# Performance work log

Hardware: AMD Instinct MI355X
Metric: run time of the kernel (lower is better)

## Reference

```python
import jax, jax.numpy as jnp
import numpy as np

B, N, L, K, C1 = 128, 300, 600, 19, 100  # batch, num_cnns, input_length, filter_size, fc hidden
PS = 7  # pool size == stride
LC = L - (K - 1)               # 582, conv output length
LP = (LC - PS) // PS + 1       # 83, pooled length
NC = 2                         # num_classes
EPS = 1e-5


def _bn(x, g, b, m, v):
    # eval-mode batchnorm, params broadcast along given axes already
    return g * (x - m) * jax.lax.rsqrt(v + EPS) + b


def setup_inputs() -> dict:
    key = jax.random.key(0)
    ks = jax.random.split(key, 20)
    f = lambda i, shape, s=0.1: (jax.random.normal(ks[i], shape, dtype=jnp.float32) * s)
    pv = lambda i, shape: (jax.random.uniform(ks[i], shape, dtype=jnp.float32) + 0.5)
    return {
        'x': jax.random.normal(ks[0], (B, 4, L), dtype=jnp.float32),
        'conv_w': f(1, (N, 4, K)), 'conv_b': f(2, (N,)),
        'bn1_g': pv(3, (N,)), 'bn1_b': f(4, (N,)), 'bn1_m': f(5, (N,)), 'bn1_v': pv(6, (N,)),
        'fc1_w': f(7, (N, C1, LP)), 'fc1_b': f(8, (N, C1)),
        'bn2_g': pv(9, (N, C1)), 'bn2_b': f(10, (N, C1)), 'bn2_m': f(11, (N, C1)), 'bn2_v': pv(12, (N, C1)),
        'fc2_w': f(13, (N, C1)), 'fc2_b': f(14, (N,)),
        'bn3_g': pv(15, (N,)), 'bn3_b': f(16, (N,)), 'bn3_m': f(17, (N,)), 'bn3_v': pv(18, (N,)),
        'final_w': f(19, (NC, N)), 'final_b': jnp.zeros((NC,), dtype=jnp.float32),
    }


def reference(x, conv_w, conv_b, bn1_g, bn1_b, bn1_m, bn1_v,
              fc1_w, fc1_b, bn2_g, bn2_b, bn2_m, bn2_v,
              fc2_w, fc2_b, bn3_g, bn3_b, bn3_m, bn3_v,
              final_w, final_b):
    # grouped conv on a repeated input == plain conv with 4 in-channels, N out-channels
    h = jax.lax.conv_general_dilated(x, conv_w, window_strides=(1,), padding='VALID',
                                     dimension_numbers=('NCH', 'OIH', 'NCH'))  # [B,N,582]
    h = h + conv_b[None, :, None]
    h = _bn(h, bn1_g[None, :, None], bn1_b[None, :, None], bn1_m[None, :, None], bn1_v[None, :, None])
    h = jnp.exp(h)
    # MaxPool1d(7,7): [B,N,582] -> [B,N,83]
    h = jax.lax.reduce_window(h, -jnp.inf, jax.lax.max,
                              window_dimensions=(1, 1, PS), window_strides=(1, 1, PS), padding='VALID')
    # grouped 1x1 conv == per-unit dense: [B,N,83] x [N,100,83] -> [B,N,100]
    h = jnp.einsum('bnp,nhp->bnh', h, fc1_w) + fc1_b[None]
    h = jax.nn.relu(_bn(h, bn2_g[None], bn2_b[None], bn2_m[None], bn2_v[None]))
    # second grouped 1x1 conv: [B,N,100] x [N,100] -> [B,N]
    h = jnp.einsum('bnh,nh->bn', h, fc2_w) + fc2_b[None]
    h = jax.nn.relu(_bn(h, bn3_g[None], bn3_b[None], bn3_m[None], bn3_v[None]))
    return h @ final_w.T + final_b  # [B,num_classes]
```

## Files before the change

kernel.cpp:

```cpp
#include <hip/hip_runtime.h>
#include <math.h>

#define EPS_ 1e-5f

__global__ __launch_bounds__(256) void kP(const float* __restrict__ fc1w,
                                          const float* __restrict__ conv_w,
                                          float* __restrict__ w1Tp,
                                          float* __restrict__ cw4) {
    const int blk = blockIdx.x, tid = threadIdx.x;
    if (blk < 300) {
        __shared__ float sm[83 * 101];
        for (int i = tid; i < 8300; i += 256) {
            const int h = i / 83, p = i - h * 83;
            sm[p * 101 + h] = fc1w[(size_t)blk * 8300 + i];
        }
        __syncthreads();
        for (int i = tid; i < 9296; i += 256) {
            const int p = i / 112, h = i - p * 112;
            w1Tp[(size_t)blk * 9296 + i] = (h < 100) ? sm[p * 101 + h] : 0.f;
        }
    } else {
        const int cq = blk - 300;
        const int c  = cq / 5;
        const int kq = cq - c * 5;
        for (int n = tid; n < 300; n += 256) {
            float4 v;
            const int k0 = 4 * kq;
            v.x = (k0 + 0 < 19) ? conv_w[n * 76 + c * 19 + k0 + 0] : 0.f;
            v.y = (k0 + 1 < 19) ? conv_w[n * 76 + c * 19 + k0 + 1] : 0.f;
            v.z = (k0 + 2 < 19) ? conv_w[n * 76 + c * 19 + k0 + 2] : 0.f;
            v.w = (k0 + 3 < 19) ? conv_w[n * 76 + c * 19 + k0 + 3] : 0.f;
            reinterpret_cast<float4*>(cw4)[(c * 5 + kq) * 300 + n] = v;
        }
    }
}

__global__ __launch_bounds__(64) void kA(
        const float* __restrict__ x,
        const float* __restrict__ cw4,
        const float* __restrict__ conv_b,
        const float* __restrict__ g1, const float* __restrict__ b1,
        const float* __restrict__ m1, const float* __restrict__ v1,
        float* __restrict__ pooled)
{
    const int id  = blockIdx.x;
    const int b   = id / 112;
    const int sub = id - b * 112;
    if (sub >= 105) return;
    const int ng  = sub / 21;
    const int pc  = sub - ng * 21;
    const int p0c = pc * 4;
    const int p0  = (p0c > 79) ? 79 : p0c;
    const int lane = threadIdx.x;
    const int n   = ng * 64 + lane;
    const int nc  = (n < 300) ? n : 299;

    const float4* w4 = reinterpret_cast<const float4*>(cw4);

    float acc[28];
    #pragma unroll
    for (int i = 0; i < 28; ++i) acc[i] = 0.f;

    #pragma unroll 1
    for (int c = 0; c < 4; ++c) {
        const float* xc = x + b * 2400 + c * 600 + 7 * p0;
        float xw[46];
        #pragma unroll
        for (int j = 0; j < 46; ++j) xw[j] = xc[j];
        #pragma unroll
        for (int kq = 0; kq < 5; ++kq) {
            const float4 wv = w4[(c * 5 + kq) * 300 + nc];
            const int ni = (kq == 4) ? 3 : 4;
            #pragma unroll
            for (int i = 0; i < ni; ++i) {
                const int k = 4 * kq + i;
                const float wvv = (i == 0) ? wv.x : (i == 1) ? wv.y
                                : (i == 2) ? wv.z : wv.w;
                #pragma unroll
                for (int p = 0; p < 4; ++p)
                    #pragma unroll
                    for (int q = 0; q < 7; ++q)
                        acc[p * 7 + q] = fmaf(xw[7 * p + q + k], wvv,
                                              acc[p * 7 + q]);
            }
        }
    }

    const float A1 = g1[nc] * rsqrtf(v1[nc] + EPS_);
    const float B1 = fmaf(A1, conv_b[nc] - m1[nc], b1[nc]);
    if (n < 300) {
        float* op = pooled + ((size_t)n * 83 + p0) * 128 + b;
        #pragma unroll
        for (int p = 0; p < 4; ++p) {
            float mx = -INFINITY;
            #pragma unroll
            for (int q = 0; q < 7; ++q)
                mx = fmaxf(mx, fmaf(A1, acc[p * 7 + q], B1));
            op[p * 128] = __expf(mx);
        }
    }
}

__global__ __launch_bounds__(256, 2) void kB(
        const float* __restrict__ pooled,
        const float* __restrict__ w1Tp,
        const float* __restrict__ fc1b,
        const float* __restrict__ g2, const float* __restrict__ b2,
        const float* __restrict__ m2, const float* __restrict__ v2,
        const float* __restrict__ fc2w,
        const float* __restrict__ fc2b,
        const float* __restrict__ g3, const float* __restrict__ b3,
        const float* __restrict__ m3, const float* __restrict__ v3,
        float* __restrict__ sout)
{
    __shared__ __align__(16) float sW[83 * 112];
    __shared__ float2 sRed[4][64];
    const int n   = blockIdx.x;
    const int tid = threadIdx.x;

    {
        const float4* src = reinterpret_cast<const float4*>(w1Tp + (size_t)n * 9296);
        float4* dst = reinterpret_cast<float4*>(sW);
        for (int i = tid; i < 2324; i += 256) dst[i] = src[i];
    }
    __syncthreads();

    const int lane = tid & 63;
    const int wv   = __builtin_amdgcn_readfirstlane(tid >> 6);
    const int h0   = wv * 28;
    const int b0   = lane * 2;

    const float* pp = pooled + (size_t)n * 83 * 128 + b0;

    float acc[28][2];
    #pragma unroll
    for (int j = 0; j < 28; ++j) { acc[j][0] = 0.f; acc[j][1] = 0.f; }

    #pragma unroll 4
    for (int p = 0; p < 83; ++p) {
        const float2 pv = *reinterpret_cast<const float2*>(pp + p * 128);
        const float* wrow = sW + p * 112 + h0;
        #pragma unroll
        for (int jq = 0; jq < 7; ++jq) {
            const float4 w = *reinterpret_cast<const float4*>(wrow + 4 * jq);
            acc[jq * 4 + 0][0] = fmaf(w.x, pv.x, acc[jq * 4 + 0][0]);
            acc[jq * 4 + 0][1] = fmaf(w.x, pv.y, acc[jq * 4 + 0][1]);
            acc[jq * 4 + 1][0] = fmaf(w.y, pv.x, acc[jq * 4 + 1][0]);
            acc[jq * 4 + 1][1] = fmaf(w.y, pv.y, acc[jq * 4 + 1][1]);
            acc[jq * 4 + 2][0] = fmaf(w.z, pv.x, acc[jq * 4 + 2][0]);
            acc[jq * 4 + 2][1] = fmaf(w.z, pv.y, acc[jq * 4 + 2][1]);
            acc[jq * 4 + 3][0] = fmaf(w.w, pv.x, acc[jq * 4 + 3][0]);
            acc[jq * 4 + 3][1] = fmaf(w.w, pv.y, acc[jq * 4 + 3][1]);
        }
    }

    const int nh = (wv < 3) ? 28 : 16;
    float p0s = 0.f, p1s = 0.f;
    for (int j = 0; j < nh; ++j) {
        const int hi = n * 100 + h0 + j;
        const float A2 = g2[hi] * rsqrtf(v2[hi] + EPS_);
        const float C2 = fmaf(A2, fc1b[hi] - m2[hi], b2[hi]);
        const float w2 = fc2w[hi];
        p0s = fmaf(fmaxf(fmaf(A2, acc[j][0], C2), 0.f), w2, p0s);
        p1s = fmaf(fmaxf(fmaf(A2, acc[j][1], C2), 0.f), w2, p1s);
    }
    sRed[wv][lane] = make_float2(p0s, p1s);
    __syncthreads();

    if (tid < 128) {
        const int l = tid >> 1, r = tid & 1;
        float s = (r == 0)
            ? (sRed[0][l].x + sRed[1][l].x + sRed[2][l].x + sRed[3][l].x)
            : (sRed[0][l].y + sRed[1][l].y + sRed[2][l].y + sRed[3][l].y);
        s += fc2b[n];
        const float A3 = g3[n] * rsqrtf(v3[n] + EPS_);
        const float z = fmaf(A3, s - m3[n], b3[n]);
        sout[n * 128 + tid] = fmaxf(z, 0.f);
    }
}

__global__ __launch_bounds__(64) void kC(
        const float* __restrict__ sout,
        const float* __restrict__ fw,
        const float* __restrict__ fb,
        float* __restrict__ out)
{
    const int b = blockIdx.x, t = threadIdx.x;
    float a0 = 0.f, a1 = 0.f;
    for (int nn = t; nn < 300; nn += 64) {
        const float v = sout[nn * 128 + b];
        a0 = fmaf(v, fw[nn], a0);
        a1 = fmaf(v, fw[300 + nn], a1);
    }
    #pragma unroll
    for (int off = 32; off > 0; off >>= 1) {
        a0 += __shfl_xor(a0, off, 64);
        a1 += __shfl_xor(a1, off, 64);
    }
    if (t == 0) {
        out[b * 2 + 0] = a0 + fb[0];
        out[b * 2 + 1] = a1 + fb[1];
    }
}

extern "C" void kernel_launch(void* const* d_in, const int* in_sizes, int n_in,
                              void* d_out, int out_size, void* d_ws, size_t ws_size,
                              hipStream_t stream) {
    const float* x      = (const float*)d_in[0];
    const float* conv_w = (const float*)d_in[1];
    const float* conv_b = (const float*)d_in[2];
    const float* g1 = (const float*)d_in[3];
    const float* b1 = (const float*)d_in[4];
    const float* m1 = (const float*)d_in[5];
    const float* v1 = (const float*)d_in[6];
    const float* fc1_w = (const float*)d_in[7];
    const float* fc1_b = (const float*)d_in[8];
    const float* g2 = (const float*)d_in[9];
    const float* b2 = (const float*)d_in[10];
    const float* m2 = (const float*)d_in[11];
    const float* v2 = (const float*)d_in[12];
    const float* fc2_w = (const float*)d_in[13];
    const float* fc2_b = (const float*)d_in[14];
    const float* g3 = (const float*)d_in[15];
    const float* b3 = (const float*)d_in[16];
    const float* m3 = (const float*)d_in[17];
    const float* v3 = (const float*)d_in[18];
    const float* fw = (const float*)d_in[19];
    const float* fb = (const float*)d_in[20];
    float* out = (float*)d_out;

    float* pooled = (float*)d_ws;
    float* w1Tp   = pooled + (size_t)300 * 83 * 128;
    float* cw4    = w1Tp + (size_t)300 * 9296;
    float* sout   = cw4 + 24000;

    kP<<<320, 256, 0, stream>>>(fc1_w, conv_w, w1Tp, cw4);
    kA<<<128 * 112, 64, 0, stream>>>(x, cw4, conv_b, g1, b1, m1, v1, pooled);
    kB<<<300, 256, 0, stream>>>(pooled, w1Tp, fc1_b, g2, b2, m2, v2,
                                fc2_w, fc2_b, g3, b3, m3, v3, sout);
    kC<<<128, 64, 0, stream>>>(sout, fw, fb, out);
}
```

Measured before the change: 186.7 us.

## Fuse fc1 weight transpose into kB and widen conv tile to six pooled outputs

The separate pre-pass that transposed fc1 weights into a padded global buffer is removed. kB now loads the raw fc1 weights and transposes them directly into shared memory, zero-filling the pad columns. This saves one global write and re-read of about 11 MB, at the cost of strided shared-memory stores in kB. Separately, each kA block now computes 6 pooled positions instead of 4, giving fewer blocks and more reuse of the x window, but more registers per thread (42 accumulators and 60 inputs).

New measurement: 183.9 us. Within noise of the previous version (-1.5%).

```diff
diff --git a/kernel.cpp b/kernel.cpp
--- a/kernel.cpp
+++ b/kernel.cpp
@@ -3,35 +3,19 @@
 
 #define EPS_ 1e-5f
 
-__global__ __launch_bounds__(256) void kP(const float* __restrict__ fc1w,
-                                          const float* __restrict__ conv_w,
-                                          float* __restrict__ w1Tp,
+__global__ __launch_bounds__(256) void kP(const float* __restrict__ conv_w,
                                           float* __restrict__ cw4) {
-    const int blk = blockIdx.x, tid = threadIdx.x;
-    if (blk < 300) {
-        __shared__ float sm[83 * 101];
-        for (int i = tid; i < 8300; i += 256) {
-            const int h = i / 83, p = i - h * 83;
-            sm[p * 101 + h] = fc1w[(size_t)blk * 8300 + i];
-        }
-        __syncthreads();
-        for (int i = tid; i < 9296; i += 256) {
-            const int p = i / 112, h = i - p * 112;
-            w1Tp[(size_t)blk * 9296 + i] = (h < 100) ? sm[p * 101 + h] : 0.f;
-        }
-    } else {
-        const int cq = blk - 300;
-        const int c  = cq / 5;
-        const int kq = cq - c * 5;
-        for (int n = tid; n < 300; n += 256) {
-            float4 v;
-            const int k0 = 4 * kq;
-            v.x = (k0 + 0 < 19) ? conv_w[n * 76 + c * 19 + k0 + 0] : 0.f;
-            v.y = (k0 + 1 < 19) ? conv_w[n * 76 + c * 19 + k0 + 1] : 0.f;
-            v.z = (k0 + 2 < 19) ? conv_w[n * 76 + c * 19 + k0 + 2] : 0.f;
-            v.w = (k0 + 3 < 19) ? conv_w[n * 76 + c * 19 + k0 + 3] : 0.f;
-            reinterpret_cast<float4*>(cw4)[(c * 5 + kq) * 300 + n] = v;
-        }
+    const int cq = blockIdx.x;
+    const int c  = cq / 5;
+    const int kq = cq - c * 5;
+    for (int n = threadIdx.x; n < 300; n += 256) {
+        float4 v;
+        const int k0 = 4 * kq;
+        v.x = (k0 + 0 < 19) ? conv_w[n * 76 + c * 19 + k0 + 0] : 0.f;
+        v.y = (k0 + 1 < 19) ? conv_w[n * 76 + c * 19 + k0 + 1] : 0.f;
+        v.z = (k0 + 2 < 19) ? conv_w[n * 76 + c * 19 + k0 + 2] : 0.f;
+        v.w = (k0 + 3 < 19) ? conv_w[n * 76 + c * 19 + k0 + 3] : 0.f;
+        reinterpret_cast<float4*>(cw4)[(c * 5 + kq) * 300 + n] = v;
     }
 }
 
@@ -44,29 +28,29 @@
         float* __restrict__ pooled)
 {
     const int id  = blockIdx.x;
-    const int b   = id / 112;
-    const int sub = id - b * 112;
-    if (sub >= 105) return;
-    const int ng  = sub / 21;
-    const int pc  = sub - ng * 21;
-    const int p0c = pc * 4;
-    const int p0  = (p0c > 79) ? 79 : p0c;
+    const int b   = id / 72;
+    const int sub = id - b * 72;
+    if (sub >= 70) return;
+    const int ng  = sub / 14;
+    const int pc  = sub - ng * 14;
+    const int p0c = pc * 6;
+    const int p0  = (p0c > 77) ? 77 : p0c;
     const int lane = threadIdx.x;
     const int n   = ng * 64 + lane;
     const int nc  = (n < 300) ? n : 299;
 
     const float4* w4 = reinterpret_cast<const float4*>(cw4);
 
-    float acc[28];
+    float acc[42];
     #pragma unroll
-    for (int i = 0; i < 28; ++i) acc[i] = 0.f;
+    for (int i = 0; i < 42; ++i) acc[i] = 0.f;
 
     #pragma unroll 1
     for (int c = 0; c < 4; ++c) {
         const float* xc = x + b * 2400 + c * 600 + 7 * p0;
-        float xw[46];
-        #pragma unroll
-        for (int j = 0; j < 46; ++j) xw[j] = xc[j];
+        float xw[60];
+        #pragma unroll
+        for (int j = 0; j < 60; ++j) xw[j] = xc[j];
         #pragma unroll
         for (int kq = 0; kq < 5; ++kq) {
             const float4 wv = w4[(c * 5 + kq) * 300 + nc];
@@ -77,7 +61,7 @@
                 const float wvv = (i == 0) ? wv.x : (i == 1) ? wv.y
                                 : (i == 2) ? wv.z : wv.w;
                 #pragma unroll
-                for (int p = 0; p < 4; ++p)
+                for (int p = 0; p < 6; ++p)
                     #pragma unroll
                     for (int q = 0; q < 7; ++q)
                         acc[p * 7 + q] = fmaf(xw[7 * p + q + k], wvv,
@@ -91,7 +75,7 @@
     if (n < 300) {
         float* op = pooled + ((size_t)n * 83 + p0) * 128 + b;
         #pragma unroll
-        for (int p = 0; p < 4; ++p) {
+        for (int p = 0; p < 6; ++p) {
             float mx = -INFINITY;
             #pragma unroll
             for (int q = 0; q < 7; ++q)
@@ -103,7 +87,7 @@
 
 __global__ __launch_bounds__(256, 2) void kB(
         const float* __restrict__ pooled,
-        const float* __restrict__ w1Tp,
+        const float* __restrict__ fc1w,
         const float* __restrict__ fc1b,
         const float* __restrict__ g2, const float* __restrict__ b2,
         const float* __restrict__ m2, const float* __restrict__ v2,
@@ -119,9 +103,15 @@
     const int tid = threadIdx.x;
 
     {
-        const float4* src = reinterpret_cast<const float4*>(w1Tp + (size_t)n * 9296);
-        float4* dst = reinterpret_cast<float4*>(sW);
-        for (int i = tid; i < 2324; i += 256) dst[i] = src[i];
+        const float* src = fc1w + (size_t)n * 8300;
+        for (int i = tid; i < 8300; i += 256) {
+            const int h = i / 83, p = i - h * 83;
+            sW[p * 112 + h] = src[i];
+        }
+        for (int i = tid; i < 996; i += 256) {
+            const int p = i / 12, h = 100 + (i - p * 12);
+            sW[p * 112 + h] = 0.f;
+        }
     }
     __syncthreads();
 
@@ -230,13 +220,12 @@
     float* out = (float*)d_out;
 
     float* pooled = (float*)d_ws;
-    float* w1Tp   = pooled + (size_t)300 * 83 * 128;
-    float* cw4    = w1Tp + (size_t)300 * 9296;
+    float* cw4    = pooled + (size_t)300 * 83 * 128;
     float* sout   = cw4 + 24000;
 
-    kP<<<320, 256, 0, stream>>>(fc1_w, conv_w, w1Tp, cw4);
-    kA<<<128 * 112, 64, 0, stream>>>(x, cw4, conv_b, g1, b1, m1, v1, pooled);
-    kB<<<300, 256, 0, stream>>>(pooled, w1Tp, fc1_b, g2, b2, m2, v2,
+    kP<<<20, 256, 0, stream>>>(conv_w, cw4);
+    kA<<<128 * 72, 64, 0, stream>>>(x, cw4, conv_b, g1, b1, m1, v1, pooled);
+    kB<<<300, 256, 0, stream>>>(pooled, fc1_w, fc1_b, g2, b2, m2, v2,
                                 fc2_w, fc2_b, g3, b3, m3, v3, sout);
     kC<<<128, 64, 0, stream>>>(sout, fw, fb, out);
 }
```
